# Kernel optimization log

Measured on AMD Instinct MI355X. Metric: run time of the kernel, lower is better.

Reference implementation:

```python
import jax, jax.numpy as jnp
import numpy as np
from jax import lax

BN_EPS = 1e-5
SP_NEAR = 2


def fps(xyz, m):
    # xyz: [b, n, c] -> indices [b, m]; deterministic start at index 0
    b, n, _ = xyz.shape
    def step(carry, _):
        dist, far = carry
        centroid = jnp.take_along_axis(xyz, far[:, None, None], axis=1)  # [b,1,c]
        d = jnp.sum((xyz - centroid) ** 2, axis=-1)                      # [b,n]
        dist = jnp.minimum(dist, d)
        return (dist, jnp.argmax(dist, axis=-1).astype(jnp.int32)), far
    init = (jnp.full((b, n), jnp.inf, xyz.dtype), jnp.zeros((b,), jnp.int32))
    _, idxs = lax.scan(step, init, None, length=m)
    return jnp.transpose(idxs)  # [b, m]


def knn(x, k):
    # x: [b, n, c] -> k nearest (incl. self) indices [b, n, k]
    sq = jnp.sum(x * x, axis=-1)
    d = sq[:, :, None] + sq[:, None, :] - 2.0 * jnp.einsum('bnc,bmc->bnm', x, x)
    return lax.top_k(-d, k)[1]


def gather_cf(x, idx):
    # channel-first index_points: x [b, c, n], idx [b, ...] -> [b, c, *idx.shape[1:]]
    b, c = x.shape[:2]
    flat = idx.reshape(b, -1)
    g = jnp.take_along_axis(x, flat[:, None, :], axis=2)
    return g.reshape((b, c) + idx.shape[1:])


def gather_cl(x, idx):
    # channel-last index_points: x [b, n, c], idx [b, ...] -> [b, *idx.shape[1:], c]
    b, c = x.shape[0], x.shape[-1]
    flat = idx.reshape(b, -1)
    g = jnp.take_along_axis(x, flat[:, :, None], axis=1)
    return g.reshape((b,) + idx.shape[1:] + (c,))


def bn_act(x, gamma, beta, nd):
    # inference-mode BatchNorm (running mean 0, var 1) + exact GELU; Dropout is identity in eval
    shp = (1, -1) + (1,) * nd
    scale = 1.0 / jnp.sqrt(1.0 + BN_EPS)
    return jax.nn.gelu(gamma.reshape(shp) * (x * scale) + beta.reshape(shp), approximate=False)


def setup_inputs() -> dict:
    key = jax.random.key(0)
    ks = jax.random.split(key, 8)
    BS, SP_IN, SP_OUT, DN_IN, DN_OUT = 128, 256, 256, 128, 128
    N_STK, N_STK_PNT, COOR = 32, 32, 32
    return {
        'sparse_fea': jax.random.normal(ks[0], (BS, SP_IN, N_STK), jnp.float32),
        'dense_fea': jax.random.normal(ks[1], (BS, DN_IN, N_STK, N_STK_PNT), jnp.float32),
        'stk_coor': jax.random.normal(ks[2], (BS, N_STK, COOR), jnp.float32),
        'n_stk_center': 16,
        'sp_w': jax.random.normal(ks[3], (SP_OUT, 2 * SP_IN), jnp.float32) * 0.02,
        'sp_b': jnp.zeros((SP_OUT,), jnp.float32),
        'sp_g': jnp.ones((SP_OUT,), jnp.float32),
        'sp_beta': jnp.zeros((SP_OUT,), jnp.float32),
        'dn_w': jax.random.normal(ks[4], (DN_OUT, 2 * DN_IN), jnp.float32) * 0.02,
        'dn_b': jnp.zeros((DN_OUT,), jnp.float32),
        'dn_g': jnp.ones((DN_OUT,), jnp.float32),
        'dn_beta': jnp.zeros((DN_OUT,), jnp.float32),
        'ds_w': jax.random.normal(ks[5], (DN_OUT, DN_IN, 1, 3), jnp.float32) * 0.05,
        'ds_b': jnp.zeros((DN_OUT,), jnp.float32),
        'ds_g': jnp.ones((DN_OUT,), jnp.float32),
        'ds_beta': jnp.zeros((DN_OUT,), jnp.float32),
    }


def reference(sparse_fea, dense_fea, stk_coor, n_stk_center,
              sp_w, sp_b, sp_g, sp_beta,
              dn_w, dn_b, dn_g, dn_beta,
              ds_w, ds_b, ds_g, ds_beta):
    bs, dn_in, n_stk, n_stk_pnt = dense_fea.shape
    fps_idx = fps(stk_coor, n_stk_center)            # [b, m]
    # --- sparse branch ---
    sc = gather_cf(sparse_fea, fps_idx)              # [b, c, m]
    knn_all = knn(stk_coor, SP_NEAR)                 # [b, n, k]
    knn_fps = gather_cl(knn_all, fps_idx)            # [b, m, k]
    sn = gather_cf(sparse_fea, knn_fps)              # [b, c, m, k]
    sa = sn - sc[:, :, :, None]
    sp_x = jnp.concatenate([sa, jnp.broadcast_to(sc[:, :, :, None], sa.shape)], axis=1)  # [b,2c,m,k]
    sp_x = jnp.einsum('bimk,oi->bomk', sp_x, sp_w) + sp_b[None, :, None, None]
    sp_x = bn_act(sp_x, sp_g, sp_beta, 2)
    sparse_out = jnp.max(sp_x, axis=3)               # [b, sp_out, m]
    # --- dense branch ---
    # 'b c s sp -> b s (sp c)'
    d_flat = jnp.transpose(dense_fea, (0, 2, 3, 1)).reshape(bs, n_stk, n_stk_pnt * dn_in)
    dc = gather_cl(d_flat, fps_idx)                  # [b, m, sp*c]
    dnb = gather_cl(d_flat, knn_fps)                 # [b, m, k, sp*c]
    da = dnb - dc[:, :, None, :]
    dcat = jnp.concatenate([da, jnp.broadcast_to(dc[:, :, None, :], da.shape)], axis=3)  # [b,m,k,2*sp*c]
    # 'b s n (sp c) -> b c s sp n' with sp=n_stk_pnt (exact torch reshape semantics)
    d5 = dcat.reshape(bs, fps_idx.shape[1], SP_NEAR, n_stk_pnt, 2 * dn_in)
    d5 = jnp.transpose(d5, (0, 4, 1, 3, 2))          # [b, 2c, m, sp, k]
    d5 = jnp.einsum('bimpn,oi->bompn', d5, dn_w) + dn_b[None, :, None, None, None]
    d5 = bn_act(d5, dn_g, dn_beta, 3)
    d4 = jnp.max(d5, axis=4)                         # [b, dn_out, m, sp]
    y = lax.conv_general_dilated(d4, ds_w, window_strides=(1, 2), padding=((0, 0), (1, 1)),
                                 dimension_numbers=('NCHW', 'OIHW', 'NCHW')) + ds_b[None, :, None, None]
    dense_out = bn_act(y, ds_g, ds_beta, 2)          # [b, dn_out, m, sp//2]
    coor_out = gather_cl(stk_coor, fps_idx)          # [b, m, coor]
    return sparse_out, dense_out, coor_out
```

## Files before the change

### kernel.cpp

```cpp
#include <hip/hip_runtime.h>


typedef unsigned short u16;
typedef unsigned int   u32;
typedef __attribute__((ext_vector_type(8))) short bf16x8;
typedef __attribute__((ext_vector_type(4))) float f32x4;

#define BN_SCALE 0.9999950000374997f

__device__ __forceinline__ float gelu_f(float x){
  return 0.5f*x*(1.0f + erff(x*0.70710678118654752f));
}
__device__ __forceinline__ u16 f2bf(float f){
  u32 x = __float_as_uint(f);
  x += 0x7fffu + ((x>>16)&1u);
  return (u16)(x>>16);
}

__global__ __launch_bounds__(256) void k_weights(
    const float* __restrict__ dn_w, const float* __restrict__ ds_w, const float* __restrict__ sp_w,
    u16* __restrict__ wdb, u16* __restrict__ wcb, u16* __restrict__ wsb)
{
  int blk = blockIdx.x, t = threadIdx.x;
  if (blk < 128){
    int w = blk*256 + t;
    int j=w&7, lane=(w>>3)&63, tile=w>>9;
    int kt=tile>>3, ot=tile&7;
    int o=ot*16+(lane&15), i=kt*32+((lane>>4)&3)*8+j;
    wdb[w] = f2bf(dn_w[o*256+i]);
  } else if (blk < 320){
    int w = (blk-128)*256 + t;
    int j=w&7, lane=(w>>3)&63, tile=w>>9;
    int kt=tile>>3, ot=tile&7;
    int o=ot*16+(lane&15), k=kt*32+((lane>>4)&3)*8+j;
    wcb[w] = f2bf(ds_w[o*384+k]);
  } else {
    int w = (blk-320)*256 + t;
    int j=w&7, lane=(w>>3)&63, tile=w>>9;
    int kt=tile>>4, ot=tile&15;
    int o=ot*16+(lane&15), i=kt*32+((lane>>4)&3)*8+j;
    wsb[w] = f2bf(sp_w[o*512+i]);
  }
}

__global__ __launch_bounds__(256) void k_fps(
    const float* __restrict__ coor,
    int* __restrict__ fps_idx, int* __restrict__ nn_idx, float* __restrict__ coor_out)
{
  int b = blockIdx.x, t = threadIdx.x;
  __shared__ float Xs[32*33];
  __shared__ float D[32*33];
  __shared__ int   s_sel[16];
  for (int i=t;i<1024;i+=256) Xs[(i>>5)*33 + (i&31)] = coor[b*1024+i];
  __syncthreads();
  #pragma unroll
  for (int k2=0;k2<4;k2++){
    int p=t+k2*256, i=p>>5, j=p&31;
    float d=0.f;
    #pragma unroll
    for (int c=0;c<32;c++){ float df=Xs[i*33+c]-Xs[j*33+c]; d+=df*df; }
    D[i*33+j]=d;
  }
  __syncthreads();
  if (t < 64){
    int j = t & 31;
    float dist = 3.0e38f;
    int far = 0;
    #pragma unroll
    for (int it=0; it<16; ++it){
      if (t==0) s_sel[it]=far;
      dist = fminf(dist, D[far*33+j]);
      float v=dist; int idx=j;
      #pragma unroll
      for (int off=16; off>=1; off>>=1){
        float v2=__shfl_xor(v,off,32); int i2=__shfl_xor(idx,off,32);
        if (v2>v || (v2==v && i2<idx)){ v=v2; idx=i2; }
      }
      far = idx;
    }
    if (t==0){
      #pragma unroll
      for (int it=0;it<16;++it) fps_idx[b*16+it]=s_sel[it];
    }
  }
  __syncthreads();
  {
    int wv=t>>6, j=t&31;
    #pragma unroll
    for (int q=0;q<4;q++){
      int it = wv*4+q, sel = s_sel[it];
      float d = D[sel*33+j];
      if (j==sel) d=3.0e38f;
      float v=d; int idx=j;
      #pragma unroll
      for (int off=16; off>=1; off>>=1){
        float v2=__shfl_xor(v,off,32); int i2=__shfl_xor(idx,off,32);
        if (v2<v || (v2==v && i2<idx)){ v=v2; idx=i2; }
      }
      if ((t&63)==0) nn_idx[b*16+it]=idx;
    }
  }
  for (int q=t;q<512;q+=256){
    int mm=q>>5, c=q&31;
    coor_out[b*512+q] = Xs[s_sel[mm]*33 + c];
  }
}

__global__ __launch_bounds__(256) void k_main(
    const float* __restrict__ sfea, const u16* __restrict__ wsb,
    const float* __restrict__ sp_b, const float* __restrict__ sp_g, const float* __restrict__ sp_be,
    const float* __restrict__ dfea, const u16* __restrict__ wdb,
    const float* __restrict__ dn_b, const float* __restrict__ dn_g, const float* __restrict__ dn_be,
    const u16* __restrict__ wcb,
    const float* __restrict__ ds_b, const float* __restrict__ ds_g, const float* __restrict__ ds_be,
    const int* __restrict__ fps_idx, const int* __restrict__ nn_idx,
    float* __restrict__ out_sp, float* __restrict__ out_dn)
{
  __shared__ char smem[16896];
  int blk=blockIdx.x;
  int t=threadIdx.x, lane=t&63, wv=t>>6, quad=lane>>4, col=lane&15;
  if (blk < 256){
    int b = ((blk>>4)<<3) | (blk&7), oh = (blk>>3)&1;
    u16*   Xb = (u16*)smem;
    float* P  = (float*)smem;
    __shared__ int SI[32];
    if (t<16){ SI[t]=fps_idx[b*16+t]&31; SI[16+t]=nn_idx[b*16+t]&31; }
    __syncthreads();
    const float* row = sfea + b*8192 + t*32;
    #pragma unroll
    for (int m=0;m<16;m++){
      float vc=row[SI[m]], vn=row[SI[16+m]];
      Xb[m*520 + t]       = f2bf(vn-vc);
      Xb[m*520 + 256 + t] = f2bf(vc);
    }
    __syncthreads();
    f32x4 accA[2]={}, accB[2]={};
    for (int kt=0;kt<8;kt++){
      bf16x8 bfr = *(const bf16x8*)&Xb[col*520 + kt*32 + quad*8];
      #pragma unroll
      for (int r=0;r<2;r++){
        int ot = oh*8 + wv + r*4;
        bf16x8 afr = *(const bf16x8*)&wsb[((kt*16+ot)*64+lane)*8];
        accA[r]=__builtin_amdgcn_mfma_f32_16x16x32_bf16(afr,bfr,accA[r],0,0,0);
      }
    }
    for (int kt=8;kt<16;kt++){
      bf16x8 bfr = *(const bf16x8*)&Xb[col*520 + kt*32 + quad*8];
      #pragma unroll
      for (int r=0;r<2;r++){
        int ot = oh*8 + wv + r*4;
        bf16x8 afr = *(const bf16x8*)&wsb[((kt*16+ot)*64+lane)*8];
        accB[r]=__builtin_amdgcn_mfma_f32_16x16x32_bf16(afr,bfr,accB[r],0,0,0);
      }
    }
    __syncthreads();
    P[t]=sp_b[t]; P[256+t]=sp_g[t]; P[512+t]=sp_be[t];
    __syncthreads();
    #pragma unroll
    for (int r=0;r<2;r++){
      #pragma unroll
      for (int reg=0;reg<4;reg++){
        int o = oh*128 + (wv+r*4)*16 + quad*4 + reg;
        float bo=P[o], go=P[256+o], be=P[512+o];
        float k1 = accA[r][reg]+accB[r][reg]+bo;
        float k0 = accB[r][reg]+bo;
        float v = fmaxf(gelu_f(go*(k1*BN_SCALE)+be), gelu_f(go*(k0*BN_SCALE)+be));
        out_sp[(b*256+o)*16 + col] = v;
      }
    }
  } else {
    int d=blk-256;
    int b = ((d>>7)<<3) | (d&7), m = (d>>3)&15;
    u16* Vb = (u16*)smem;
    u16* Bc = (u16*)smem;
    float* P = (float*)(smem+12544);
    int mi = b*16+m;
    int ci=fps_idx[mi]&31, ni=nn_idx[mi]&31;
    const float* Db = dfea + b*131072;
    for (int fp=t; fp<2048; fp+=256){
      int c=fp>>4, xp=fp&15, x=xp*2;
      float2 fc = *(const float2*)(Db + c*1024 + ci*32 + x);
      float2 fn = *(const float2*)(Db + c*1024 + ni*32 + x);
      Vb[xp*264 + c]            = f2bf(fn.x-fc.x);
      Vb[(16+xp)*264 + c]       = f2bf(fc.x);
      Vb[xp*264 + 128 + c]      = f2bf(fn.y-fc.y);
      Vb[(16+xp)*264 + 128 + c] = f2bf(fc.y);
    }
    __syncthreads();
    f32x4 acc[2][2]={};
    for (int kt=0;kt<8;kt++){
      bf16x8 b0 = *(const bf16x8*)&Vb[ col     *264 + kt*32 + quad*8];
      bf16x8 b1 = *(const bf16x8*)&Vb[(16+col) *264 + kt*32 + quad*8];
      #pragma unroll
      for (int r=0;r<2;r++){
        int ot=wv+r*4;
        bf16x8 afr = *(const bf16x8*)&wdb[((kt*8+ot)*64+lane)*8];
        acc[r][0]=__builtin_amdgcn_mfma_f32_16x16x32_bf16(afr,b0,acc[r][0],0,0,0);
        acc[r][1]=__builtin_amdgcn_mfma_f32_16x16x32_bf16(afr,b1,acc[r][1],0,0,0);
      }
    }
    __syncthreads();
    for (int q=t; q<3136; q+=256) ((u32*)Bc)[q]=0u;
    if (t<128){
      float b0=dn_b[t], g0=dn_g[t], e0=dn_be[t];
      P[t]=b0; P[128+t]=g0; P[256+t]=e0;
      P[384+t]=ds_b[t]; P[512+t]=ds_g[t]; P[640+t]=ds_be[t];
      P[768+t]=gelu_f(g0*(b0*BN_SCALE)+e0);
    }
    __syncthreads();
    #pragma unroll
    for (int r=0;r<2;r++){
      #pragma unroll
      for (int pt=0;pt<2;pt++){
        #pragma unroll
        for (int reg=0;reg<4;reg++){
          int o = (wv+r*4)*16 + quad*4 + reg;
          int p = pt*16 + col;
          float bo=P[o], go=P[128+o], be=P[256+o];
          float val = gelu_f(go*((acc[r][pt][reg]+bo)*BN_SCALE)+be);
          if (pt==0) val = fmaxf(val, P[768+o]);
          u16 bv = f2bf(val);
          if (p&1){
            Bc[((p-1)>>1)*392 + o*3 + 2] = bv;
            if (p<31) Bc[((p+1)>>1)*392 + o*3 + 0] = bv;
          } else {
            Bc[(p>>1)*392 + o*3 + 1] = bv;
          }
        }
      }
    }
    __syncthreads();
    f32x4 cacc[2]={};
    for (int kt=0;kt<12;kt++){
      bf16x8 bfr = *(const bf16x8*)&Bc[col*392 + kt*32 + quad*8];
      #pragma unroll
      for (int r=0;r<2;r++){
        int ot=wv+r*4;
        bf16x8 afr = *(const bf16x8*)&wcb[((kt*8+ot)*64+lane)*8];
        cacc[r]=__builtin_amdgcn_mfma_f32_16x16x32_bf16(afr,bfr,cacc[r],0,0,0);
      }
    }
    #pragma unroll
    for (int r=0;r<2;r++){
      #pragma unroll
      for (int reg=0;reg<4;reg++){
        int o = (wv+r*4)*16 + quad*4 + reg;
        float cb=P[384+o], go=P[512+o], be=P[640+o];
        float val = gelu_f(go*((cacc[r][reg]+cb)*BN_SCALE)+be);
        out_dn[(b*128+o)*256 + m*16 + col] = val;
      }
    }
  }
}

extern "C" void kernel_launch(void* const* d_in, const int* in_sizes, int n_in,
                              void* d_out, int out_size, void* d_ws, size_t ws_size,
                              hipStream_t stream) {
  const float* sparse_fea = (const float*)d_in[0];
  const float* dense_fea  = (const float*)d_in[1];
  const float* stk_coor   = (const float*)d_in[2];
  const float* sp_w  = (const float*)d_in[4];
  const float* sp_b  = (const float*)d_in[5];
  const float* sp_g  = (const float*)d_in[6];
  const float* sp_be = (const float*)d_in[7];
  const float* dn_w  = (const float*)d_in[8];
  const float* dn_b  = (const float*)d_in[9];
  const float* dn_g  = (const float*)d_in[10];
  const float* dn_be = (const float*)d_in[11];
  const float* ds_w  = (const float*)d_in[12];
  const float* ds_b  = (const float*)d_in[13];
  const float* ds_g  = (const float*)d_in[14];
  const float* ds_be = (const float*)d_in[15];

  float* out = (float*)d_out;
  int* fps_idx = (int*)d_ws;
  int* nn_idx  = fps_idx + 2048;
  u16* wdb = (u16*)((char*)d_ws + 16384);
  u16* wcb = (u16*)((char*)d_ws + 81920);
  u16* wsb = (u16*)((char*)d_ws + 180224);

  k_fps    <<<128, 256, 0, stream>>>(stk_coor, fps_idx, nn_idx, out + 4718592);
  k_weights<<<832, 256, 0, stream>>>(dn_w, ds_w, sp_w, wdb, wcb, wsb);
  k_main   <<<2304, 256, 0, stream>>>(sparse_fea, wsb, sp_b, sp_g, sp_be,
                                      dense_fea, wdb, dn_b, dn_g, dn_be,
                                      wcb, ds_b, ds_g, ds_be,
                                      fps_idx, nn_idx, out, out + 524288);
}
```

Before: 172.1 us.

## Merge FPS into weight-prep kernel and process two items per main block

The FPS/kNN kernel is folded into the weight-conversion kernel, so one launch does both. The main kernel now handles two batches per sparse block (each block computes both output halves) and two centroids per dense block, so every weight fragment load feeds twice as many MFMAs. Dense gathers move to float4 loads, and only the padding entries of the conv buffer are zeroed. In exchange, blocks use more shared memory and registers, which lowers occupancy and halves the grid from 2304 to 1088 blocks.

```diff
diff --git a/kernel.cpp b/kernel.cpp
--- a/kernel.cpp
+++ b/kernel.cpp
@@ -17,9 +17,11 @@
   return (u16)(x>>16);
 }
 
-__global__ __launch_bounds__(256) void k_weights(
+__global__ __launch_bounds__(256) void k_prep(
     const float* __restrict__ dn_w, const float* __restrict__ ds_w, const float* __restrict__ sp_w,
-    u16* __restrict__ wdb, u16* __restrict__ wcb, u16* __restrict__ wsb)
+    const float* __restrict__ coor,
+    u16* __restrict__ wdb, u16* __restrict__ wcb, u16* __restrict__ wsb,
+    int* __restrict__ fps_idx, int* __restrict__ nn_idx, float* __restrict__ coor_out)
 {
   int blk = blockIdx.x, t = threadIdx.x;
   if (blk < 128){
@@ -34,75 +36,70 @@
     int kt=tile>>3, ot=tile&7;
     int o=ot*16+(lane&15), k=kt*32+((lane>>4)&3)*8+j;
     wcb[w] = f2bf(ds_w[o*384+k]);
-  } else {
+  } else if (blk < 832){
     int w = (blk-320)*256 + t;
     int j=w&7, lane=(w>>3)&63, tile=w>>9;
     int kt=tile>>4, ot=tile&15;
     int o=ot*16+(lane&15), i=kt*32+((lane>>4)&3)*8+j;
     wsb[w] = f2bf(sp_w[o*512+i]);
-  }
-}
-
-__global__ __launch_bounds__(256) void k_fps(
-    const float* __restrict__ coor,
-    int* __restrict__ fps_idx, int* __restrict__ nn_idx, float* __restrict__ coor_out)
-{
-  int b = blockIdx.x, t = threadIdx.x;
-  __shared__ float Xs[32*33];
-  __shared__ float D[32*33];
-  __shared__ int   s_sel[16];
-  for (int i=t;i<1024;i+=256) Xs[(i>>5)*33 + (i&31)] = coor[b*1024+i];
-  __syncthreads();
-  #pragma unroll
-  for (int k2=0;k2<4;k2++){
-    int p=t+k2*256, i=p>>5, j=p&31;
-    float d=0.f;
-    #pragma unroll
-    for (int c=0;c<32;c++){ float df=Xs[i*33+c]-Xs[j*33+c]; d+=df*df; }
-    D[i*33+j]=d;
-  }
-  __syncthreads();
-  if (t < 64){
-    int j = t & 31;
-    float dist = 3.0e38f;
-    int far = 0;
-    #pragma unroll
-    for (int it=0; it<16; ++it){
-      if (t==0) s_sel[it]=far;
-      dist = fminf(dist, D[far*33+j]);
-      float v=dist; int idx=j;
-      #pragma unroll
-      for (int off=16; off>=1; off>>=1){
-        float v2=__shfl_xor(v,off,32); int i2=__shfl_xor(idx,off,32);
-        if (v2>v || (v2==v && i2<idx)){ v=v2; idx=i2; }
-      }
-      far = idx;
-    }
-    if (t==0){
-      #pragma unroll
-      for (int it=0;it<16;++it) fps_idx[b*16+it]=s_sel[it];
-    }
-  }
-  __syncthreads();
-  {
-    int wv=t>>6, j=t&31;
-    #pragma unroll
-    for (int q=0;q<4;q++){
-      int it = wv*4+q, sel = s_sel[it];
-      float d = D[sel*33+j];
-      if (j==sel) d=3.0e38f;
-      float v=d; int idx=j;
-      #pragma unroll
-      for (int off=16; off>=1; off>>=1){
-        float v2=__shfl_xor(v,off,32); int i2=__shfl_xor(idx,off,32);
-        if (v2<v || (v2==v && i2<idx)){ v=v2; idx=i2; }
-      }
-      if ((t&63)==0) nn_idx[b*16+it]=idx;
-    }
-  }
-  for (int q=t;q<512;q+=256){
-    int mm=q>>5, c=q&31;
-    coor_out[b*512+q] = Xs[s_sel[mm]*33 + c];
+  } else {
+    int b = blk - 832;
+    __shared__ float Xs[32*33];
+    __shared__ float D[32*33];
+    __shared__ int   s_sel[16];
+    for (int i=t;i<1024;i+=256) Xs[(i>>5)*33 + (i&31)] = coor[b*1024+i];
+    __syncthreads();
+    #pragma unroll
+    for (int k2=0;k2<4;k2++){
+      int p=t+k2*256, i=p>>5, j=p&31;
+      float d=0.f;
+      #pragma unroll
+      for (int c=0;c<32;c++){ float df=Xs[i*33+c]-Xs[j*33+c]; d+=df*df; }
+      D[i*33+j]=d;
+    }
+    __syncthreads();
+    if (t < 64){
+      int j = t & 31;
+      float dist = 3.0e38f;
+      int far = 0;
+      #pragma unroll
+      for (int it=0; it<16; ++it){
+        if (t==0) s_sel[it]=far;
+        dist = fminf(dist, D[far*33+j]);
+        float v=dist; int idx=j;
+        #pragma unroll
+        for (int off=16; off>=1; off>>=1){
+          float v2=__shfl_xor(v,off,32); int i2=__shfl_xor(idx,off,32);
+          if (v2>v || (v2==v && i2<idx)){ v=v2; idx=i2; }
+        }
+        far = idx;
+      }
+      if (t==0){
+        #pragma unroll
+        for (int it=0;it<16;++it) fps_idx[b*16+it]=s_sel[it];
+      }
+    }
+    __syncthreads();
+    {
+      int wv=t>>6, j=t&31;
+      #pragma unroll
+      for (int q=0;q<4;q++){
+        int it = wv*4+q, sel = s_sel[it];
+        float d = D[sel*33+j];
+        if (j==sel) d=3.0e38f;
+        float v=d; int idx=j;
+        #pragma unroll
+        for (int off=16; off>=1; off>>=1){
+          float v2=__shfl_xor(v,off,32); int i2=__shfl_xor(idx,off,32);
+          if (v2<v || (v2==v && i2<idx)){ v=v2; idx=i2; }
+        }
+        if ((t&63)==0) nn_idx[b*16+it]=idx;
+      }
+    }
+    for (int q=t;q<512;q+=256){
+      int mm=q>>5, c=q&31;
+      coor_out[b*512+q] = Xs[s_sel[mm]*33 + c];
+    }
   }
 }
 
@@ -116,138 +113,166 @@
     const int* __restrict__ fps_idx, const int* __restrict__ nn_idx,
     float* __restrict__ out_sp, float* __restrict__ out_dn)
 {
-  __shared__ char smem[16896];
+  __shared__ char smem[36352];
+  __shared__ int SI[64];
   int blk=blockIdx.x;
   int t=threadIdx.x, lane=t&63, wv=t>>6, quad=lane>>4, col=lane&15;
-  if (blk < 256){
-    int b = ((blk>>4)<<3) | (blk&7), oh = (blk>>3)&1;
+  if (blk < 64){
+    int b0 = blk*2;
     u16*   Xb = (u16*)smem;
-    float* P  = (float*)smem;
-    __shared__ int SI[32];
-    if (t<16){ SI[t]=fps_idx[b*16+t]&31; SI[16+t]=nn_idx[b*16+t]&31; }
-    __syncthreads();
-    const float* row = sfea + b*8192 + t*32;
-    #pragma unroll
-    for (int m=0;m<16;m++){
-      float vc=row[SI[m]], vn=row[SI[16+m]];
-      Xb[m*520 + t]       = f2bf(vn-vc);
-      Xb[m*520 + 256 + t] = f2bf(vc);
-    }
-    __syncthreads();
-    f32x4 accA[2]={}, accB[2]={};
-    for (int kt=0;kt<8;kt++){
-      bf16x8 bfr = *(const bf16x8*)&Xb[col*520 + kt*32 + quad*8];
-      #pragma unroll
-      for (int r=0;r<2;r++){
-        int ot = oh*8 + wv + r*4;
-        bf16x8 afr = *(const bf16x8*)&wsb[((kt*16+ot)*64+lane)*8];
-        accA[r]=__builtin_amdgcn_mfma_f32_16x16x32_bf16(afr,bfr,accA[r],0,0,0);
-      }
-    }
-    for (int kt=8;kt<16;kt++){
-      bf16x8 bfr = *(const bf16x8*)&Xb[col*520 + kt*32 + quad*8];
-      #pragma unroll
-      for (int r=0;r<2;r++){
-        int ot = oh*8 + wv + r*4;
-        bf16x8 afr = *(const bf16x8*)&wsb[((kt*16+ot)*64+lane)*8];
-        accB[r]=__builtin_amdgcn_mfma_f32_16x16x32_bf16(afr,bfr,accB[r],0,0,0);
-      }
-    }
-    __syncthreads();
+    float* P  = (float*)(smem+33280);
+    if (t<64){
+      int bb=t>>5, q=t&31, b=b0+bb;
+      SI[t] = ((q<16) ? fps_idx[b*16+q] : nn_idx[b*16+(q-16)]) & 31;
+    }
     P[t]=sp_b[t]; P[256+t]=sp_g[t]; P[512+t]=sp_be[t];
     __syncthreads();
     #pragma unroll
-    for (int r=0;r<2;r++){
-      #pragma unroll
-      for (int reg=0;reg<4;reg++){
-        int o = oh*128 + (wv+r*4)*16 + quad*4 + reg;
-        float bo=P[o], go=P[256+o], be=P[512+o];
-        float k1 = accA[r][reg]+accB[r][reg]+bo;
-        float k0 = accB[r][reg]+bo;
-        float v = fmaxf(gelu_f(go*(k1*BN_SCALE)+be), gelu_f(go*(k0*BN_SCALE)+be));
-        out_sp[(b*256+o)*16 + col] = v;
+    for (int bb=0;bb<2;bb++){
+      const float* row = sfea + (b0+bb)*8192 + t*32;
+      #pragma unroll
+      for (int m=0;m<16;m++){
+        float vc=row[SI[bb*32+m]], vn=row[SI[bb*32+16+m]];
+        Xb[bb*8320 + m*520 + t]       = f2bf(vn-vc);
+        Xb[bb*8320 + m*520 + 256 + t] = f2bf(vc);
+      }
+    }
+    __syncthreads();
+    #pragma unroll
+    for (int oh=0;oh<2;oh++){
+      f32x4 accA[2][2]={}, accB[2][2]={};
+      #pragma unroll
+      for (int kt=0;kt<16;kt++){
+        bf16x8 bf0 = *(const bf16x8*)&Xb[        col*520 + kt*32 + quad*8];
+        bf16x8 bf1 = *(const bf16x8*)&Xb[8320 +  col*520 + kt*32 + quad*8];
+        #pragma unroll
+        for (int r=0;r<2;r++){
+          bf16x8 afr = *(const bf16x8*)&wsb[((kt*16 + oh*8 + wv + r*4)*64+lane)*8];
+          if (kt<8){
+            accA[0][r]=__builtin_amdgcn_mfma_f32_16x16x32_bf16(afr,bf0,accA[0][r],0,0,0);
+            accA[1][r]=__builtin_amdgcn_mfma_f32_16x16x32_bf16(afr,bf1,accA[1][r],0,0,0);
+          } else {
+            accB[0][r]=__builtin_amdgcn_mfma_f32_16x16x32_bf16(afr,bf0,accB[0][r],0,0,0);
+            accB[1][r]=__builtin_amdgcn_mfma_f32_16x16x32_bf16(afr,bf1,accB[1][r],0,0,0);
+          }
+        }
+      }
+      #pragma unroll
+      for (int bb=0;bb<2;bb++){
+        #pragma unroll
+        for (int r=0;r<2;r++){
+          #pragma unroll
+          for (int reg=0;reg<4;reg++){
+            int o = oh*128 + (wv+r*4)*16 + quad*4 + reg;
+            float bo=P[o], go=P[256+o], be=P[512+o];
+            float k1 = accA[bb][r][reg]+accB[bb][r][reg]+bo;
+            float k0 = accB[bb][r][reg]+bo;
+            float v = fmaxf(gelu_f(go*(k1*BN_SCALE)+be), gelu_f(go*(k0*BN_SCALE)+be));
+            out_sp[((b0+bb)*256+o)*16 + col] = v;
+          }
+        }
       }
     }
   } else {
-    int d=blk-256;
-    int b = ((d>>7)<<3) | (d&7), m = (d>>3)&15;
+    int d=blk-64;
+    int b = ((d>>6)<<3) | (d&7), m0 = ((d>>3)&7)*2;
     u16* Vb = (u16*)smem;
     u16* Bc = (u16*)smem;
-    float* P = (float*)(smem+12544);
-    int mi = b*16+m;
-    int ci=fps_idx[mi]&31, ni=nn_idx[mi]&31;
+    float* P = (float*)(smem+25088);
+    int ci0=fps_idx[b*16+m0]&31,   ni0=nn_idx[b*16+m0]&31;
+    int ci1=fps_idx[b*16+m0+1]&31, ni1=nn_idx[b*16+m0+1]&31;
     const float* Db = dfea + b*131072;
-    for (int fp=t; fp<2048; fp+=256){
-      int c=fp>>4, xp=fp&15, x=xp*2;
-      float2 fc = *(const float2*)(Db + c*1024 + ci*32 + x);
-      float2 fn = *(const float2*)(Db + c*1024 + ni*32 + x);
-      Vb[xp*264 + c]            = f2bf(fn.x-fc.x);
-      Vb[(16+xp)*264 + c]       = f2bf(fc.x);
-      Vb[xp*264 + 128 + c]      = f2bf(fn.y-fc.y);
-      Vb[(16+xp)*264 + 128 + c] = f2bf(fc.y);
-    }
-    __syncthreads();
-    f32x4 acc[2][2]={};
+    #pragma unroll
+    for (int ld=0; ld<8; ld++){
+      int fp = t + ld*256;
+      int mi = fp>>10, idx = fp&1023, c = idx>>3, x = (idx&7)*4;
+      int ci = mi ? ci1 : ci0, ni = mi ? ni1 : ni0;
+      float4 fc4 = *(const float4*)(Db + c*1024 + ci*32 + x);
+      float4 fn4 = *(const float4*)(Db + c*1024 + ni*32 + x);
+      u16* VbM = Vb + mi*8448;
+      #pragma unroll
+      for (int e=0;e<4;e++){
+        int xx=x+e, dp=xx&1, p=xx>>1;
+        float fc=((const float*)&fc4)[e], fn=((const float*)&fn4)[e];
+        VbM[p*264 + dp*128 + c]      = f2bf(fn-fc);
+        VbM[(16+p)*264 + dp*128 + c] = f2bf(fc);
+      }
+    }
+    __syncthreads();
+    f32x4 acc[2][4]={};
+    #pragma unroll
     for (int kt=0;kt<8;kt++){
-      bf16x8 b0 = *(const bf16x8*)&Vb[ col     *264 + kt*32 + quad*8];
-      bf16x8 b1 = *(const bf16x8*)&Vb[(16+col) *264 + kt*32 + quad*8];
+      bf16x8 bfr[4];
+      #pragma unroll
+      for (int mi=0;mi<2;mi++)
+        #pragma unroll
+        for (int pt=0;pt<2;pt++)
+          bfr[mi*2+pt] = *(const bf16x8*)&Vb[mi*8448 + (pt*16+col)*264 + kt*32 + quad*8];
       #pragma unroll
       for (int r=0;r<2;r++){
-        int ot=wv+r*4;
-        bf16x8 afr = *(const bf16x8*)&wdb[((kt*8+ot)*64+lane)*8];
-        acc[r][0]=__builtin_amdgcn_mfma_f32_16x16x32_bf16(afr,b0,acc[r][0],0,0,0);
-        acc[r][1]=__builtin_amdgcn_mfma_f32_16x16x32_bf16(afr,b1,acc[r][1],0,0,0);
-      }
-    }
-    __syncthreads();
-    for (int q=t; q<3136; q+=256) ((u32*)Bc)[q]=0u;
+        bf16x8 afr = *(const bf16x8*)&wdb[((kt*8+wv+r*4)*64+lane)*8];
+        #pragma unroll
+        for (int q=0;q<4;q++)
+          acc[r][q]=__builtin_amdgcn_mfma_f32_16x16x32_bf16(afr,bfr[q],acc[r][q],0,0,0);
+      }
+    }
+    __syncthreads();
     if (t<128){
-      float b0=dn_b[t], g0=dn_g[t], e0=dn_be[t];
-      P[t]=b0; P[128+t]=g0; P[256+t]=e0;
+      float b0v=dn_b[t], g0=dn_g[t], e0=dn_be[t];
+      P[t]=b0v; P[128+t]=g0; P[256+t]=e0;
       P[384+t]=ds_b[t]; P[512+t]=ds_g[t]; P[640+t]=ds_be[t];
-      P[768+t]=gelu_f(g0*(b0*BN_SCALE)+e0);
-    }
+      P[768+t]=gelu_f(g0*(b0v*BN_SCALE)+e0);
+    }
+    { int mi=t>>7, o=t&127; Bc[mi*6272 + o*3] = 0; }
     __syncthreads();
     #pragma unroll
     for (int r=0;r<2;r++){
       #pragma unroll
-      for (int pt=0;pt<2;pt++){
+      for (int mi=0;mi<2;mi++){
+        u16* BcM = Bc + mi*6272;
+        #pragma unroll
+        for (int pt=0;pt<2;pt++){
+          #pragma unroll
+          for (int reg=0;reg<4;reg++){
+            int o = (wv+r*4)*16 + quad*4 + reg;
+            int p = pt*16 + col;
+            float bo=P[o], go=P[128+o], be=P[256+o];
+            float val = gelu_f(go*((acc[r][mi*2+pt][reg]+bo)*BN_SCALE)+be);
+            if (pt==0) val = fmaxf(val, P[768+o]);
+            u16 bv = f2bf(val);
+            if (p&1){
+              BcM[((p-1)>>1)*392 + o*3 + 2] = bv;
+              if (p<31) BcM[((p+1)>>1)*392 + o*3 + 0] = bv;
+            } else {
+              BcM[(p>>1)*392 + o*3 + 1] = bv;
+            }
+          }
+        }
+      }
+    }
+    __syncthreads();
+    f32x4 cacc[2][2]={};
+    #pragma unroll
+    for (int kt=0;kt<12;kt++){
+      bf16x8 cb0 = *(const bf16x8*)&Bc[       col*392 + kt*32 + quad*8];
+      bf16x8 cb1 = *(const bf16x8*)&Bc[6272 + col*392 + kt*32 + quad*8];
+      #pragma unroll
+      for (int r=0;r<2;r++){
+        bf16x8 afr = *(const bf16x8*)&wcb[((kt*8+wv+r*4)*64+lane)*8];
+        cacc[r][0]=__builtin_amdgcn_mfma_f32_16x16x32_bf16(afr,cb0,cacc[r][0],0,0,0);
+        cacc[r][1]=__builtin_amdgcn_mfma_f32_16x16x32_bf16(afr,cb1,cacc[r][1],0,0,0);
+      }
+    }
+    #pragma unroll
+    for (int r=0;r<2;r++){
+      #pragma unroll
+      for (int mi=0;mi<2;mi++){
         #pragma unroll
         for (int reg=0;reg<4;reg++){
           int o = (wv+r*4)*16 + quad*4 + reg;
-          int p = pt*16 + col;
-          float bo=P[o], go=P[128+o], be=P[256+o];
-          float val = gelu_f(go*((acc[r][pt][reg]+bo)*BN_SCALE)+be);
-          if (pt==0) val = fmaxf(val, P[768+o]);
-          u16 bv = f2bf(val);
-          if (p&1){
-            Bc[((p-1)>>1)*392 + o*3 + 2] = bv;
-            if (p<31) Bc[((p+1)>>1)*392 + o*3 + 0] = bv;
-          } else {
-            Bc[(p>>1)*392 + o*3 + 1] = bv;
-          }
-        }
-      }
-    }
-    __syncthreads();
-    f32x4 cacc[2]={};
-    for (int kt=0;kt<12;kt++){
-      bf16x8 bfr = *(const bf16x8*)&Bc[col*392 + kt*32 + quad*8];
-      #pragma unroll
-      for (int r=0;r<2;r++){
-        int ot=wv+r*4;
-        bf16x8 afr = *(const bf16x8*)&wcb[((kt*8+ot)*64+lane)*8];
-        cacc[r]=__builtin_amdgcn_mfma_f32_16x16x32_bf16(afr,bfr,cacc[r],0,0,0);
-      }
-    }
-    #pragma unroll
-    for (int r=0;r<2;r++){
-      #pragma unroll
-      for (int reg=0;reg<4;reg++){
-        int o = (wv+r*4)*16 + quad*4 + reg;
-        float cb=P[384+o], go=P[512+o], be=P[640+o];
-        float val = gelu_f(go*((cacc[r][reg]+cb)*BN_SCALE)+be);
-        out_dn[(b*128+o)*256 + m*16 + col] = val;
+          float val = gelu_f(P[512+o]*((cacc[r][mi][reg]+P[384+o])*BN_SCALE)+P[640+o]);
+          out_dn[(b*128+o)*256 + (m0+mi)*16 + col] = val;
+        }
       }
     }
   }
@@ -279,10 +304,10 @@
   u16* wcb = (u16*)((char*)d_ws + 81920);
   u16* wsb = (u16*)((char*)d_ws + 180224);
 
-  k_fps    <<<128, 256, 0, stream>>>(stk_coor, fps_idx, nn_idx, out + 4718592);
-  k_weights<<<832, 256, 0, stream>>>(dn_w, ds_w, sp_w, wdb, wcb, wsb);
-  k_main   <<<2304, 256, 0, stream>>>(sparse_fea, wsb, sp_b, sp_g, sp_be,
-                                      dense_fea, wdb, dn_b, dn_g, dn_be,
-                                      wcb, ds_b, ds_g, ds_be,
-                                      fps_idx, nn_idx, out, out + 524288);
-}
+  k_prep<<<960, 256, 0, stream>>>(dn_w, ds_w, sp_w, stk_coor,
+                                  wdb, wcb, wsb, fps_idx, nn_idx, out + 4718592);
+  k_main<<<1088, 256, 0, stream>>>(sparse_fea, wsb, sp_b, sp_g, sp_be,
+                                   dense_fea, wdb, dn_b, dn_g, dn_be,
+                                   wcb, ds_b, ds_g, ds_be,
+                                   fps_idx, nn_idx, out, out + 524288);
+}
```

Result: faster. 167.3 us (-2.7%).
